# Optimization experiments

Measured on AMD Instinct MI355X. Metric: run time of the kernel, lower is better.

The kernel has to match this reference:

```python
import jax, jax.numpy as jnp
import numpy as np

STRIDES = {"p3": 8, "p4": 16, "p5": 32}
SHAPES = {"p3": (100, 152), "p4": (50, 76), "p5": (25, 38)}
STRIDE_SCALE = 4
ASPECT_RATIOS = (0.5, 1.0, 2.0)
SCALE_CLAMP = float(np.log(224.0 / 8.0))
TOPK = 2000


def fpn_location_coords(level):
    H, W = SHAPES[level]
    s = STRIDES[level]
    # NOTE: original code uses arange(feat_shape[2]) for x and feat_shape[3] for y,
    # with meshgrid(y_vals, x_vals); replicate exactly.
    x_vals = s * (jnp.arange(H, dtype=jnp.float32) + 0.5)
    y_vals = s * (jnp.arange(W, dtype=jnp.float32) + 0.5)
    y_grid, x_grid = jnp.meshgrid(y_vals, x_vals, indexing="ij")
    return jnp.stack([x_grid.reshape(-1), y_grid.reshape(-1)], axis=1)  # (H*W, 2)


def generate_anchors(locations, level):
    s = STRIDES[level]
    anchor_size = STRIDE_SCALE * s
    area = float(anchor_size) ** 2
    boxes = []
    for ar in ASPECT_RATIOS:
        w = (area / ar) ** 0.5
        h = area / w
        half = jnp.array([w, h], dtype=jnp.float32) * 0.5
        tl = locations - half
        br = locations + half
        boxes.append(jnp.concatenate([tl, br], axis=1))  # (HW, 4)
    boxes = jnp.stack(boxes, axis=1)  # (HW, A, 4)
    return boxes.reshape(-1, 4)


def apply_deltas(deltas, anchors):
    d = deltas
    dxy = d[:, :2]
    dwh = jnp.minimum(d[:, 2:], SCALE_CLAMP)
    centers = jnp.stack([(anchors[:, 0] + anchors[:, 2]) * 0.5,
                         (anchors[:, 1] + anchors[:, 3]) * 0.5], axis=1)
    dims = jnp.stack([anchors[:, 2] - anchors[:, 0],
                      anchors[:, 3] - anchors[:, 1]], axis=1)
    new_c = centers + dims * dxy
    new_d = dims * jnp.exp(dwh)
    return jnp.concatenate([new_c - 0.5 * new_d, new_c + 0.5 * new_d], axis=1)


def iou(b1, b2):
    # b1: (M,4), b2: (N,4) -> (M,N)
    xl = jnp.maximum(b1[:, None, 0], b2[None, :, 0])
    yl = jnp.maximum(b1[:, None, 1], b2[None, :, 1])
    xr = jnp.minimum(b1[:, None, 2], b2[None, :, 2])
    yr = jnp.minimum(b1[:, None, 3], b2[None, :, 3])
    inter = jnp.clip(xr - xl, 0.0) * jnp.clip(yr - yl, 0.0)
    a1 = (b1[:, 2] - b1[:, 0]) * (b1[:, 3] - b1[:, 1])
    a2 = (b2[:, 2] - b2[:, 0]) * (b2[:, 3] - b2[:, 1])
    return inter / (a1[:, None] + a2[None, :] - inter)


def setup_inputs() -> dict:
    key = jax.random.key(0)
    ks = jax.random.split(key, 6)
    d = {}
    d["feat_p3"] = jax.random.normal(ks[0], (1, 256, 100, 152), jnp.float32)
    d["feat_p4"] = jax.random.normal(ks[1], (1, 256, 50, 76), jnp.float32)
    d["feat_p5"] = jax.random.normal(ks[2], (1, 256, 25, 38), jnp.float32)
    d["deltas_p3"] = jax.random.normal(ks[3], (45600, 4), jnp.float32) * 0.1
    d["deltas_p4"] = jax.random.normal(ks[4], (11400, 4), jnp.float32) * 0.1
    d["deltas_p5"] = jax.random.normal(ks[5], (2850, 4), jnp.float32) * 0.1
    return d


def reference(feat_p3, feat_p4, feat_p5, deltas_p3, deltas_p4, deltas_p5):
    deltas = {"p3": deltas_p3, "p4": deltas_p4, "p5": deltas_p5}
    boxes_all = []
    anchors_all = []
    for level in ("p3", "p4", "p5"):
        locs = fpn_location_coords(level)
        anchors = generate_anchors(locs, level)
        boxes = apply_deltas(deltas[level], anchors)
        boxes_all.append(boxes)
        anchors_all.append(anchors)
    boxes = jnp.concatenate(boxes_all, axis=0)      # (59850, 4)
    anchors = jnp.concatenate(anchors_all, axis=0)  # (59850, 4)
    # proposal scoring proxy: score by box area magnitude of first TOPK slice
    proposals = boxes[:TOPK]
    ious = iou(proposals, anchors)  # (2000, 59850)
    max_iou = jnp.max(ious, axis=0)  # (59850,)
    return boxes, anchors, max_iou


if __name__ == "__main__":
    out = reference(**setup_inputs())
    print([o.shape for o in out])
```

## Files before the change

### kernel.cpp

```cpp
#include <hip/hip_runtime.h>
#include <math.h>

#define NTOT      59850
#define NPROP     2000
#define ANCH_OFF  239400
#define MIOU_OFF  478800
#define NCHUNK    32
#define CS        64
#define GXI       16
#define BUILD_PER 120

struct BuildConsts {
    float hw[3][3];
    float hh[3][3];
    float clampv;
};

__device__ __forceinline__ float4 make_box(float x, float y, float hwv, float hhv,
                                           float4 d, float clampv)
{
    float ax0 = x - hwv, ay0 = y - hhv;
    float ax1 = x + hwv, ay1 = y + hhv;
    float w  = ax1 - ax0, h = ay1 - ay0;
    float cx = (ax0 + ax1) * 0.5f, cy = (ay0 + ay1) * 0.5f;
    float dwx = fminf(d.z, clampv), dwy = fminf(d.w, clampv);
    float ncx = cx + w * d.x, ncy = cy + h * d.y;
    float nw  = w * expf(dwx), nh = h * expf(dwy);
    return make_float4(ncx - 0.5f * nw, ncy - 0.5f * nh,
                       ncx + 0.5f * nw, ncy + 0.5f * nh);
}

__device__ __forceinline__ void anchor_from_id(int g, const BuildConsts& C,
    float& x, float& y, float& hwv, float& hhv)
{
    if (g < 45600) {
        int loc = g / 3, r = g - loc * 3;
        int i = loc / 100, j = loc - i * 100;
        x = 8.f * ((float)j + 0.5f);  y = 8.f * ((float)i + 0.5f);
        hwv = C.hw[0][r]; hhv = C.hh[0][r];
    } else if (g < 57000) {
        int a = g - 45600;
        int loc = a / 3, r = a - loc * 3;
        int i = loc / 50, j = loc - i * 50;
        x = 16.f * ((float)j + 0.5f); y = 16.f * ((float)i + 0.5f);
        hwv = C.hw[1][r]; hhv = C.hh[1][r];
    } else {
        int a = g - 57000;
        int loc = a / 3, r = a - loc * 3;
        int i = loc / 25, j = loc - i * 25;
        x = 32.f * ((float)j + 0.5f); y = 32.f * ((float)i + 0.5f);
        hwv = C.hw[2][r]; hhv = C.hh[2][r];
    }
}

#define RECT(L, S, NX, NY, i0v, j0v, njv, nv)                                  \
    int i0v, j0v, njv, nv;                                                     \
    {                                                                          \
        float hwm = C.hw[L][0], hhm = C.hh[L][2];                              \
        int j0t = (int)floorf((bb.x - hwm) * (1.0f / S) - 0.5f) - 1;           \
        int j1t = (int)ceilf ((bb.z + hwm) * (1.0f / S) - 0.5f) + 1;           \
        int i0t = (int)floorf((bb.y - hhm) * (1.0f / S) - 0.5f) - 1;           \
        int i1t = (int)ceilf ((bb.w + hhm) * (1.0f / S) - 0.5f) + 1;           \
        j0t = max(0, j0t); j1t = min(NX - 1, j1t);                             \
        i0t = max(0, i0t); i1t = min(NY - 1, i1t);                             \
        int njt = j1t - j0t + 1, nit = i1t - i0t + 1;                          \
        if (njt < 0) njt = 0;                                                  \
        if (nit < 0) nit = 0;                                                  \
        i0v = i0t; j0v = j0t; njv = njt; nv = nit * njt * 3;                   \
    }

__global__ __launch_bounds__(256) void rpn_kernel(
    const float4* __restrict__ d3,
    const float4* __restrict__ d4,
    const float4* __restrict__ d5,
    float* __restrict__ out,
    BuildConsts C)
{
    __shared__ float4 Pb[CS];
    __shared__ float  Pa[CS];
    __shared__ float4 bbS;

    int tid = threadIdx.x;
    int bx  = blockIdx.x;
    int cy  = blockIdx.y;
    float* miou = out + MIOU_OFF;

    int gb = (cy * GXI + bx) * BUILD_PER + tid;
    if (tid < BUILD_PER && gb < NTOT) {
        const float4* dl; int a;
        if (gb < 45600)      { dl = d3; a = gb; }
        else if (gb < 57000) { dl = d4; a = gb - 45600; }
        else                 { dl = d5; a = gb - 57000; }
        float x, y, hwv, hhv;
        anchor_from_id(gb, C, x, y, hwv, hhv);
        ((float4*)out)[gb] = make_box(x, y, hwv, hhv, dl[a], C.clampv);
        ((float4*)(out + ANCH_OFF))[gb] =
            make_float4(x - hwv, y - hhv, x + hwv, y + hhv);
        atomicMax((int*)(miou + gb), 0);
    }

    if (tid < CS) {
        int p = cy * CS + tid;
        p = p < NPROP ? p : NPROP - 1;
        int loc = p / 3, r = p - loc * 3;
        int i = loc / 100, j = loc - i * 100;
        float x = 8.0f * ((float)j + 0.5f);
        float y = 8.0f * ((float)i + 0.5f);
        float4 b = make_box(x, y, C.hw[0][r], C.hh[0][r], d3[p], C.clampv);
        Pb[tid] = b;
        Pa[tid] = (b.z - b.x) * (b.w - b.y);
        float bx0 = b.x, by0 = b.y, bx1 = b.z, by1 = b.w;
        #pragma unroll
        for (int m = 32; m; m >>= 1) {
            bx0 = fminf(bx0, __shfl_xor(bx0, m));
            by0 = fminf(by0, __shfl_xor(by0, m));
            bx1 = fmaxf(bx1, __shfl_xor(bx1, m));
            by1 = fmaxf(by1, __shfl_xor(by1, m));
        }
        if (tid == 0) bbS = make_float4(bx0, by0, bx1, by1);
    }
    __syncthreads();
    float4 bb = bbS;

    RECT(0,  8.f, 100, 152, i0L0, j0L0, njL0, nL0)
    RECT(1, 16.f,  50,  76, i0L1, j0L1, njL1, nL1)
    RECT(2, 32.f,  25,  38, i0L2, j0L2, njL2, nL2)
    int b1 = nL0, b2 = nL0 + nL1, NL = b2 + nL2;

    for (int pos = bx * 256 + tid; pos < NL; pos += GXI * 256) {
        bool ge1 = pos >= b1, ge2 = pos >= b2;
        int t      = pos - (ge2 ? b2 : (ge1 ? b1 : 0));
        unsigned nj = (unsigned)(ge2 ? njL2 : (ge1 ? njL1 : njL0));
        int i0s    = ge2 ? i0L2 : (ge1 ? i0L1 : i0L0);
        int j0s    = ge2 ? j0L2 : (ge1 ? j0L1 : j0L0);
        float s    = ge2 ? 32.f : (ge1 ? 16.f : 8.f);
        int nx     = ge2 ? 25 : (ge1 ? 50 : 100);
        int gbase  = ge2 ? 57000 : (ge1 ? 45600 : 0);

        unsigned tu  = (unsigned)t;
        unsigned loc = tu / 3u;
        int r        = (int)(tu - loc * 3u);
        unsigned irow = loc / nj;
        unsigned jcol = loc - irow * nj;
        int i = i0s + (int)irow, j = j0s + (int)jcol;

        float x = s * ((float)j + 0.5f);
        float y = s * ((float)i + 0.5f);
        float hwA = ge2 ? C.hw[2][0] : (ge1 ? C.hw[1][0] : C.hw[0][0]);
        float hwB = ge2 ? C.hw[2][1] : (ge1 ? C.hw[1][1] : C.hw[0][1]);
        float hwC = ge2 ? C.hw[2][2] : (ge1 ? C.hw[1][2] : C.hw[0][2]);
        float hhA = ge2 ? C.hh[2][0] : (ge1 ? C.hh[1][0] : C.hh[0][0]);
        float hhB = ge2 ? C.hh[2][1] : (ge1 ? C.hh[1][1] : C.hh[0][1]);
        float hhC = ge2 ? C.hh[2][2] : (ge1 ? C.hh[1][2] : C.hh[0][2]);
        float hwv = (r == 0) ? hwA : ((r == 1) ? hwB : hwC);
        float hhv = (r == 0) ? hhA : ((r == 1) ? hhB : hhC);

        float ax0 = x - hwv, ay0 = y - hhv;
        float ax1 = x + hwv, ay1 = y + hhv;
        float a2  = (2.0f * hwv) * (2.0f * hhv);

        float Ib = 0.0f, Sb = 1.0f;
        #pragma unroll 8
        for (int p = 0; p < CS; ++p) {
            float4 b  = Pb[p];
            float  pa = Pa[p];
            float xl = fmaxf(b.x, ax0);
            float yl = fmaxf(b.y, ay0);
            float xr = fminf(b.z, ax1);
            float yr = fminf(b.w, ay1);
            float iw = fmaxf(xr - xl, 0.0f);
            float ih = fmaxf(yr - yl, 0.0f);
            float inter = iw * ih;
            float S = pa + a2;
            bool better = inter * Sb > Ib * S;
            Ib = better ? inter : Ib;
            Sb = better ? S     : Sb;
        }
        if (Ib > 0.0f) {
            float m = Ib / (Sb - Ib);
            int g = gbase + (i * nx + j) * 3 + r;
            atomicMax((int*)(miou + g), __float_as_int(m));
        }
    }
}

extern "C" void kernel_launch(void* const* d_in, const int* in_sizes, int n_in,
                              void* d_out, int out_size, void* d_ws, size_t ws_size,
                              hipStream_t stream) {
    const float4* d3 = (const float4*)d_in[3];
    const float4* d4 = (const float4*)d_in[4];
    const float4* d5 = (const float4*)d_in[5];
    float* out = (float*)d_out;

    BuildConsts C;
    const double sArr[3]  = {8.0, 16.0, 32.0};
    const double arArr[3] = {0.5, 1.0, 2.0};
    for (int l = 0; l < 3; ++l) {
        double as   = 4.0 * sArr[l];
        double area = as * as;
        for (int rr = 0; rr < 3; ++rr) {
            double w = sqrt(area / arArr[rr]);
            double h = area / w;
            C.hw[l][rr] = (float)w * 0.5f;
            C.hh[l][rr] = (float)h * 0.5f;
        }
    }
    C.clampv = (float)log(224.0 / 8.0);

    rpn_kernel<<<dim3(GXI, NCHUNK), 256, 0, stream>>>(d3, d4, d5, out, C);
}
```

Measured before the change: 19.64 us.

## Replace atomicMax IoU reduction with per-chunk partials and a separate reduce kernel

Each proposal chunk now writes its per-anchor max IoU into its own workspace slice, along with the anchor rectangle it covered, instead of doing a global atomicMax. A second kernel reads these rectangles and takes the max across the 32 chunk slices for each anchor. This removes the atomic contention and the zero-initialisation atomics. In exchange it adds a second launch and extra workspace traffic (32×NTOT floats of possible reads and writes).

```diff
diff --git a/kernel.cpp b/kernel.cpp
--- a/kernel.cpp
+++ b/kernel.cpp
@@ -9,6 +9,7 @@
 #define CS        64
 #define GXI       16
 #define BUILD_PER 120
+#define PART_OFF  1024
 
 struct BuildConsts {
     float hw[3][3];
@@ -53,8 +54,8 @@
     }
 }
 
-#define RECT(L, S, NX, NY, i0v, j0v, njv, nv)                                  \
-    int i0v, j0v, njv, nv;                                                     \
+#define RECT(L, S, NX, NY, i0v, j0v, niv, njv, nv)                             \
+    int i0v, j0v, niv, njv, nv;                                                \
     {                                                                          \
         float hwm = C.hw[L][0], hhm = C.hh[L][2];                              \
         int j0t = (int)floorf((bb.x - hwm) * (1.0f / S) - 0.5f) - 1;           \
@@ -66,14 +67,16 @@
         int njt = j1t - j0t + 1, nit = i1t - i0t + 1;                          \
         if (njt < 0) njt = 0;                                                  \
         if (nit < 0) nit = 0;                                                  \
-        i0v = i0t; j0v = j0t; njv = njt; nv = nit * njt * 3;                   \
-    }
-
-__global__ __launch_bounds__(256) void rpn_kernel(
+        i0v = i0t; j0v = j0t; niv = nit; njv = njt; nv = nit * njt * 3;        \
+    }
+
+__global__ __launch_bounds__(256) void rpn_partial_kernel(
     const float4* __restrict__ d3,
     const float4* __restrict__ d4,
     const float4* __restrict__ d5,
     float* __restrict__ out,
+    int*   __restrict__ ws_i,
+    float* __restrict__ ws_f,
     BuildConsts C)
 {
     __shared__ float4 Pb[CS];
@@ -83,7 +86,6 @@
     int tid = threadIdx.x;
     int bx  = blockIdx.x;
     int cy  = blockIdx.y;
-    float* miou = out + MIOU_OFF;
 
     int gb = (cy * GXI + bx) * BUILD_PER + tid;
     if (tid < BUILD_PER && gb < NTOT) {
@@ -96,7 +98,6 @@
         ((float4*)out)[gb] = make_box(x, y, hwv, hhv, dl[a], C.clampv);
         ((float4*)(out + ANCH_OFF))[gb] =
             make_float4(x - hwv, y - hhv, x + hwv, y + hhv);
-        atomicMax((int*)(miou + gb), 0);
     }
 
     if (tid < CS) {
@@ -122,10 +123,17 @@
     __syncthreads();
     float4 bb = bbS;
 
-    RECT(0,  8.f, 100, 152, i0L0, j0L0, njL0, nL0)
-    RECT(1, 16.f,  50,  76, i0L1, j0L1, njL1, nL1)
-    RECT(2, 32.f,  25,  38, i0L2, j0L2, njL2, nL2)
+    RECT(0,  8.f, 100, 152, i0L0, j0L0, niL0, njL0, nL0)
+    RECT(1, 16.f,  50,  76, i0L1, j0L1, niL1, njL1, nL1)
+    RECT(2, 32.f,  25,  38, i0L2, j0L2, niL2, njL2, nL2)
+    if (bx == 0 && tid == 0) {
+        int b = cy * 12;
+        ws_i[b + 0] = i0L0; ws_i[b + 1] = j0L0; ws_i[b + 2]  = niL0; ws_i[b + 3]  = njL0;
+        ws_i[b + 4] = i0L1; ws_i[b + 5] = j0L1; ws_i[b + 6]  = niL1; ws_i[b + 7]  = njL1;
+        ws_i[b + 8] = i0L2; ws_i[b + 9] = j0L2; ws_i[b + 10] = niL2; ws_i[b + 11] = njL2;
+    }
     int b1 = nL0, b2 = nL0 + nL1, NL = b2 + nL2;
+    float* part = ws_f + PART_OFF + cy * NTOT;
 
     for (int pos = bx * 256 + tid; pos < NL; pos += GXI * 256) {
         bool ge1 = pos >= b1, ge2 = pos >= b2;
@@ -176,12 +184,44 @@
             Ib = better ? inter : Ib;
             Sb = better ? S     : Sb;
         }
-        if (Ib > 0.0f) {
-            float m = Ib / (Sb - Ib);
-            int g = gbase + (i * nx + j) * 3 + r;
-            atomicMax((int*)(miou + g), __float_as_int(m));
-        }
-    }
+        int g = gbase + (i * nx + j) * 3 + r;
+        part[g] = (Ib > 0.0f) ? (Ib / (Sb - Ib)) : 0.0f;
+    }
+}
+
+__global__ __launch_bounds__(256) void rpn_reduce_kernel(
+    const int*   __restrict__ ws_i,
+    const float* __restrict__ ws_f,
+    float* __restrict__ miou)
+{
+    __shared__ int R[NCHUNK * 12];
+    for (int k = threadIdx.x; k < NCHUNK * 12; k += 256) R[k] = ws_i[k];
+    __syncthreads();
+
+    int g = blockIdx.x * 256 + threadIdx.x;
+    if (g >= NTOT) return;
+
+    int lev, i, j;
+    if (g < 45600) {
+        int loc = g / 3; lev = 0; i = loc / 100; j = loc - i * 100;
+    } else if (g < 57000) {
+        int loc = (g - 45600) / 3; lev = 1; i = loc / 50; j = loc - i * 50;
+    } else {
+        int loc = (g - 57000) / 3; lev = 2; i = loc / 25; j = loc - i * 25;
+    }
+
+    const float* part = ws_f + PART_OFF;
+    float acc = 0.0f;
+    #pragma unroll 8
+    for (int cy = 0; cy < NCHUNK; ++cy) {
+        int b  = cy * 12 + lev * 4;
+        int i0 = R[b], j0 = R[b + 1], ni = R[b + 2], nj = R[b + 3];
+        if ((unsigned)(i - i0) < (unsigned)ni &&
+            (unsigned)(j - j0) < (unsigned)nj) {
+            acc = fmaxf(acc, part[cy * NTOT + g]);
+        }
+    }
+    miou[g] = acc;
 }
 
 extern "C" void kernel_launch(void* const* d_in, const int* in_sizes, int n_in,
@@ -207,5 +247,8 @@
     }
     C.clampv = (float)log(224.0 / 8.0);
 
-    rpn_kernel<<<dim3(GXI, NCHUNK), 256, 0, stream>>>(d3, d4, d5, out, C);
-}
+    rpn_partial_kernel<<<dim3(GXI, NCHUNK), 256, 0, stream>>>(
+        d3, d4, d5, out, (int*)d_ws, (float*)d_ws, C);
+    rpn_reduce_kernel<<<dim3((NTOT + 255) / 256), 256, 0, stream>>>(
+        (const int*)d_ws, (const float*)d_ws, out + MIOU_OFF);
+}
```

Measured after the change: 31.64 us. +61.1%, slower.
